# Performance work log

Measured on AMD Instinct MI355X. Metric: run time of the kernel, lower is better.

## Reference

```python
import jax, jax.numpy as jnp
import numpy as np

B, N, D = 256, 196, 768  # batch, num_patches (14x14 grid), patch_dim (16*16*3)


def setup_inputs() -> dict:
    key = jax.random.key(0)
    k1, k2 = jax.random.split(key)
    features = jax.random.normal(k1, (B, N, D), dtype=jnp.float32)
    position_logits = jax.random.normal(k2, (B, N, N), dtype=jnp.float32)
    return {"features": features, "position_logits": position_logits}


def _rearrange_patches(patches, pos):
    # Deterministic gather form: for each target slot p, take the LARGEST j with
    # pos[i, j] == p, else leave the zero-init.
    b, n, d = patches.shape
    j_ids = jnp.arange(n, dtype=jnp.int32)
    match = pos[:, :, None] == jnp.arange(n)[None, None, :]          # [B, j, p]
    winner = jnp.max(jnp.where(match, j_ids[None, :, None], -1), axis=1)  # [B, p]
    gathered = jnp.take_along_axis(patches, jnp.clip(winner, 0)[:, :, None], axis=1)
    return jnp.where(winner[:, :, None] >= 0, gathered, jnp.zeros((), patches.dtype))


def reference(features, position_logits):
    b, n, d = features.shape
    g = int(n ** 0.5)
    # _get_position_predictions: argmax / max-softmax over dim=1 (position classes)
    pos = jnp.argmax(position_logits, axis=1)                         # [B, N] int
    confidence = jnp.max(jax.nn.softmax(position_logits, axis=1), axis=1)  # [B, N]
    # _rearrange_patches (scatter by predicted position)
    patches = _rearrange_patches(features, pos)
    # _smooth_edges: 3-tap average over interior patch indices, reading originals
    mid = (patches[:, :-2] + patches[:, 1:-1] + patches[:, 2:]) / 3.0
    patches = jnp.concatenate([patches[:, :1], mid, patches[:, -1:]], axis=1)
    # _reconstruct_image: [B, g, g, D] -> [B, D, g, g]
    img = patches.reshape(b, g, g, d).transpose(0, 3, 1, 2)
    return img, confidence
```

## Files before the change

### kernel.cpp

```cpp
#include <hip/hip_runtime.h>
#include <math.h>

#define BB 256
#define NN 196
#define DD 768
#define TDK 32
#define PSTRIDE 204

typedef float f32x4 __attribute__((ext_vector_type(4)));

__global__ __launch_bounds__(1024) void pos_conf_kernel(
    const float* __restrict__ logits,
    float* __restrict__ conf_out,
    int* __restrict__ winner_out)
{
    const int b  = blockIdx.x;
    const int t  = threadIdx.x;
    const int g  = t >> 8;
    const int jj = t & 255;

    __shared__ float sm[4][256];
    __shared__ float ss[4][256];
    __shared__ int   si[4][256];
    __shared__ int   winner_s[256];

    if (t < NN) winner_s[t] = -1;

    if (jj < NN) {
        const float* col = logits + (size_t)b * NN * NN + (size_t)(49 * g) * NN + jj;
        float m = -INFINITY, s = 0.0f;
        int idx = 0;
        const int i0 = 49 * g;
        #pragma unroll 7
        for (int i = 0; i < 49; ++i) {
            const float x = col[(size_t)i * NN];
            const float mn = fmaxf(m, x);
            idx = (x > m) ? (i0 + i) : idx;
            s = s * __expf(m - mn) + __expf(x - mn);
            m = mn;
        }
        sm[g][jj] = m; ss[g][jj] = s; si[g][jj] = idx;
    }
    __syncthreads();

    if (t < NN) {
        const int j = t;
        float m = -INFINITY;
        int idx = 0;
        #pragma unroll
        for (int gg = 0; gg < 4; ++gg) {
            const float mg = sm[gg][j];
            if (mg > m) { m = mg; idx = si[gg][j]; }
        }
        float s = 0.0f;
        #pragma unroll
        for (int gg = 0; gg < 4; ++gg)
            s += ss[gg][j] * __expf(sm[gg][j] - m);
        conf_out[b * NN + j] = 1.0f / s;
        atomicMax(&winner_s[idx], j);
    }
    __syncthreads();
    if (t < NN) winner_out[b * NN + t] = winner_s[t];
}

__global__ __launch_bounds__(256) void rearrange_kernel(
    const float* __restrict__ features,
    const int* __restrict__ winner,
    float* __restrict__ img)
{
    const int b  = blockIdx.y;
    const int d0 = blockIdx.x * TDK;
    const int t  = threadIdx.x;

    __shared__ float tile[TDK][PSTRIDE];

    const float* fb = features + (size_t)b * NN * DD;
    const int* wb = winner + b * NN;

    int w[7];
    #pragma unroll
    for (int i = 0; i < 7; ++i) {
        const int r = (t >> 3) + 32 * i;
        w[i] = (r < NN) ? wb[r] : -1;
    }

    const int d4 = (t & 7) * 4;
    #pragma unroll
    for (int i = 0; i < 7; ++i) {
        const int r = (t >> 3) + 32 * i;
        if (r < NN) {
            float4 v = make_float4(0.f, 0.f, 0.f, 0.f);
            if (w[i] >= 0)
                v = *reinterpret_cast<const float4*>(fb + (size_t)w[i] * DD + d0 + d4);
            tile[d4 + 0][r] = v.x;
            tile[d4 + 1][r] = v.y;
            tile[d4 + 2][r] = v.z;
            tile[d4 + 3][r] = v.w;
        }
    }
    __syncthreads();

    #pragma unroll
    for (int it = 0; it < 7; ++it) {
        const int q = t + 256 * it;
        if (q < TDK * 49) {
            const int d = q / 49;
            const int c = q - 49 * d;
            const int p0 = 4 * c;
            const float4 ctr = *reinterpret_cast<const float4*>(&tile[d][p0]);
            const float left  = tile[d][p0 > 0 ? p0 - 1 : 0];
            const float right = tile[d][p0 + 4 < NN ? p0 + 4 : NN - 1];
            f32x4 o;
            o.x = (p0 == 0)          ? ctr.x : (left  + ctr.x + ctr.y) * (1.0f / 3.0f);
            o.y = (ctr.x + ctr.y + ctr.z) * (1.0f / 3.0f);
            o.z = (ctr.y + ctr.z + ctr.w) * (1.0f / 3.0f);
            o.w = (p0 + 3 == NN - 1) ? ctr.w : (ctr.z + ctr.w + right) * (1.0f / 3.0f);
            float* dst = img + (size_t)b * DD * NN + (size_t)(d0 + d) * NN + p0;
            __builtin_nontemporal_store(o, reinterpret_cast<f32x4*>(dst));
        }
    }
}

extern "C" void kernel_launch(void* const* d_in, const int* in_sizes, int n_in,
                              void* d_out, int out_size, void* d_ws, size_t ws_size,
                              hipStream_t stream) {
    const float* features = (const float*)d_in[0];
    const float* logits   = (const float*)d_in[1];

    float* out  = (float*)d_out;
    float* img  = out;
    float* conf = out + (size_t)BB * DD * NN;
    int*   winner = (int*)d_ws;

    pos_conf_kernel<<<BB, 1024, 0, stream>>>(logits, conf, winner);

    dim3 grid(DD / TDK, BB);
    rearrange_kernel<<<grid, 256, 0, stream>>>(features, winner, img);
}
```

Measured before the change: 52.96 us.

## Vectorize logits column scan with float4 loads across 16 wave row-groups

```diff
diff --git a/kernel.cpp b/kernel.cpp
--- a/kernel.cpp
+++ b/kernel.cpp
@@ -6,6 +6,7 @@
 #define DD 768
 #define TDK 32
 #define PSTRIDE 204
+#define NW 16
 
 typedef float f32x4 __attribute__((ext_vector_type(4)));
 
@@ -14,32 +15,47 @@
     float* __restrict__ conf_out,
     int* __restrict__ winner_out)
 {
-    const int b  = blockIdx.x;
-    const int t  = threadIdx.x;
-    const int g  = t >> 8;
-    const int jj = t & 255;
+    const int b = blockIdx.x;
+    const int t = threadIdx.x;
+    const int w = t >> 6;
+    const int l = t & 63;
 
-    __shared__ float sm[4][256];
-    __shared__ float ss[4][256];
-    __shared__ int   si[4][256];
-    __shared__ int   winner_s[256];
+    __shared__ float sm[NW][NN];
+    __shared__ float ss[NW][NN];
+    __shared__ int   si[NW][NN];
+    __shared__ int   winner_s[NN];
 
     if (t < NN) winner_s[t] = -1;
 
-    if (jj < NN) {
-        const float* col = logits + (size_t)b * NN * NN + (size_t)(49 * g) * NN + jj;
-        float m = -INFINITY, s = 0.0f;
-        int idx = 0;
-        const int i0 = 49 * g;
-        #pragma unroll 7
-        for (int i = 0; i < 49; ++i) {
-            const float x = col[(size_t)i * NN];
-            const float mn = fmaxf(m, x);
-            idx = (x > m) ? (i0 + i) : idx;
-            s = s * __expf(m - mn) + __expf(x - mn);
+    const int i0 = (49 * w) >> 2;
+    const int i1 = (49 * (w + 1)) >> 2;
+
+    if (l < 49) {
+        const float* base = logits + (size_t)b * NN * NN + 4 * l;
+        f32x4 m = {-INFINITY, -INFINITY, -INFINITY, -INFINITY};
+        f32x4 s = {0.f, 0.f, 0.f, 0.f};
+        int4 idx = make_int4(0, 0, 0, 0);
+        #pragma unroll 4
+        for (int i = i0; i < i1; ++i) {
+            const f32x4 x = *reinterpret_cast<const f32x4*>(base + (size_t)i * NN);
+            f32x4 mn;
+            mn.x = fmaxf(m.x, x.x); mn.y = fmaxf(m.y, x.y);
+            mn.z = fmaxf(m.z, x.z); mn.w = fmaxf(m.w, x.w);
+            idx.x = (x.x > m.x) ? i : idx.x;
+            idx.y = (x.y > m.y) ? i : idx.y;
+            idx.z = (x.z > m.z) ? i : idx.z;
+            idx.w = (x.w > m.w) ? i : idx.w;
+            s.x = s.x * __expf(m.x - mn.x) + __expf(x.x - mn.x);
+            s.y = s.y * __expf(m.y - mn.y) + __expf(x.y - mn.y);
+            s.z = s.z * __expf(m.z - mn.z) + __expf(x.z - mn.z);
+            s.w = s.w * __expf(m.w - mn.w) + __expf(x.w - mn.w);
             m = mn;
         }
-        sm[g][jj] = m; ss[g][jj] = s; si[g][jj] = idx;
+        const int c = 4 * l;
+        sm[w][c + 0] = m.x; ss[w][c + 0] = s.x; si[w][c + 0] = idx.x;
+        sm[w][c + 1] = m.y; ss[w][c + 1] = s.y; si[w][c + 1] = idx.y;
+        sm[w][c + 2] = m.z; ss[w][c + 2] = s.z; si[w][c + 2] = idx.z;
+        sm[w][c + 3] = m.w; ss[w][c + 3] = s.w; si[w][c + 3] = idx.w;
     }
     __syncthreads();
 
@@ -48,14 +64,14 @@
         float m = -INFINITY;
         int idx = 0;
         #pragma unroll
-        for (int gg = 0; gg < 4; ++gg) {
-            const float mg = sm[gg][j];
-            if (mg > m) { m = mg; idx = si[gg][j]; }
+        for (int ww = 0; ww < NW; ++ww) {
+            const float mg = sm[ww][j];
+            if (mg > m) { m = mg; idx = si[ww][j]; }
         }
         float s = 0.0f;
         #pragma unroll
-        for (int gg = 0; gg < 4; ++gg)
-            s += ss[gg][j] * __expf(sm[gg][j] - m);
+        for (int ww = 0; ww < NW; ++ww)
+            s += ss[ww][j] * __expf(sm[ww][j] - m);
         conf_out[b * NN + j] = 1.0f / s;
         atomicMax(&winner_s[idx], j);
     }
```

New measurement: 53.65 us. No clear change (+1.3%).
